# Kernel tuning notes

Measured on AMD Instinct MI355X. Metric: run time of the kernel, lower is better.

The kernel has to match this reference:

```python
import jax, jax.numpy as jnp
import numpy as np
from jax import lax

NB_W = 8  # weight bits
NB_A = 8  # activation bits
BN_EPS = 1e-3


def quant_weight(w, bits=NB_W):
    # symmetric per-tensor weight quantization with straight-through estimator
    qmax = 2.0 ** (bits - 1) - 1.0
    scale = jnp.max(jnp.abs(w)) / qmax
    wq = jnp.clip(jnp.round(w / scale), -qmax, qmax) * scale
    return w + lax.stop_gradient(wq - w)


def act_quant(x, alpha, bits=NB_A):
    # PACT-style: clip to [0, alpha], uniform quantize to 2^bits-1 levels, STE on round
    qmax = 2.0 ** bits - 1.0
    a = alpha.reshape(())
    xc = jnp.clip(x, 0.0, a)
    s = a / qmax
    xq = jnp.round(xc / s) * s
    return xc + lax.stop_gradient(xq - xc)


def bn_eval(x, gamma, beta, mean, var):
    inv = gamma / jnp.sqrt(var + BN_EPS)
    return x * inv[None, :, None, None] + (beta - mean * inv)[None, :, None, None]


def conv2d(x, w):
    return lax.conv_general_dilated(x, w, (1, 1), 'VALID',
                                    dimension_numbers=('NCHW', 'OIHW', 'NCHW'))


def setup_inputs() -> dict:
    ks = jax.random.split(jax.random.key(0), 8)
    B, C, H, W = 256, 768, 17, 17
    inp = {
        'act': jax.random.normal(ks[0], (B, C, H, W), jnp.float32),
        'alpha_in': jnp.ones((1,), jnp.float32),
        'conv0_w': jax.random.normal(ks[1], (128, 768, 1, 1), jnp.float32) * 0.05,
        'bn0_gamma': jnp.ones((128,), jnp.float32),
        'bn0_beta': jnp.zeros((128,), jnp.float32),
        'bn0_mean': jnp.zeros((128,), jnp.float32),
        'bn0_var': jnp.ones((128,), jnp.float32),
        'alpha0': jnp.full((1,), 8.0, jnp.float32),
        'conv1_w': jax.random.normal(ks[2], (768, 128, 5, 5), jnp.float32) * 0.01,
        'bn1_gamma': jnp.ones((768,), jnp.float32),
        'bn1_beta': jnp.zeros((768,), jnp.float32),
        'bn1_mean': jnp.zeros((768,), jnp.float32),
        'bn1_var': jnp.ones((768,), jnp.float32),
        'alpha1': jnp.full((1,), 8.0, jnp.float32),
        'fc_w': jax.random.normal(ks[3], (1000, 768), jnp.float32) * 0.001,
        'fc_b': jnp.zeros((1000,), jnp.float32),
    }
    return inp


def reference(act, alpha_in, conv0_w, bn0_gamma, bn0_beta, bn0_mean, bn0_var, alpha0,
              conv1_w, bn1_gamma, bn1_beta, bn1_mean, bn1_var, alpha1, fc_w, fc_b):
    # avg_pool k=5 s=3 VALID: 17x17 -> 5x5
    x = lax.reduce_window(act, 0.0, lax.add, (1, 1, 5, 5), (1, 1, 3, 3), 'VALID') / 25.0
    # conv0: quantized 1x1 conv 768->128, BN, ReLU, ACT_Q
    x = conv2d(x, quant_weight(conv0_w))
    x = jax.nn.relu(bn_eval(x, bn0_gamma, bn0_beta, bn0_mean, bn0_var))
    x = act_quant(x, alpha0)
    # conv1: quantized 5x5 conv 128->768 on 5x5 -> 1x1, BN, ReLU, ACT_Q
    x = conv2d(x, quant_weight(conv1_w))
    x = jax.nn.relu(bn_eval(x, bn1_gamma, bn1_beta, bn1_mean, bn1_var))
    x = act_quant(x, alpha1)
    # adaptive avg pool to 1x1 (already 1x1) + flatten
    x = jnp.mean(x, axis=(2, 3))  # [B, 768]
    # quantized linear head
    return x @ quant_weight(fc_w).T + fc_b
```

## Files before the change

kernel.cpp:

```cpp
#include <hip/hip_runtime.h>

#define NB 256
#define NC 768
#define HW 289
#define NP 25
#define OC0 128
#define K1 3200
#define NO 1000
#define M0 6400

#define OFF_MX    0
#define OFF_W0T   256
#define OFF_POOL  (OFF_W0T + 786432)
#define OFF_A0K   (OFF_POOL + 39321600)
#define OFF_W1R   (OFF_A0K + 819200)
#define OFF_SUMR1 (OFF_W1R + 2457600)
#define OFF_A1K   (OFF_SUMR1 + 4096)
#define OFF_FCR   (OFF_A1K + 196608)
#define OFF_SUMFC (OFF_FCR + 768000)

#if __has_builtin(__builtin_amdgcn_sdot4)
__device__ __forceinline__ int DOT4(unsigned a, unsigned b, int c) {
    return __builtin_amdgcn_sdot4((int)a, (int)b, c, false);
}
#else
__device__ __forceinline__ int DOT4(unsigned a, unsigned b, int c) {
    #pragma unroll
    for (int q = 0; q < 4; ++q)
        c += (int)(char)(a >> (8*q)) * (int)(char)(b >> (8*q));
    return c;
}
#endif

__global__ void k_init(unsigned* mx) {
    if (threadIdx.x < 3) mx[threadIdx.x] = 0u;
}

__global__ void k_absmax(const float* __restrict__ w, int n, unsigned* __restrict__ out) {
    float m = 0.f;
    for (int i = blockIdx.x * blockDim.x + threadIdx.x; i < n; i += gridDim.x * blockDim.x)
        m = fmaxf(m, fabsf(w[i]));
    #pragma unroll
    for (int off = 32; off; off >>= 1) m = fmaxf(m, __shfl_down(m, off));
    __shared__ float sm[4];
    if ((threadIdx.x & 63) == 0) sm[threadIdx.x >> 6] = m;
    __syncthreads();
    if (threadIdx.x == 0)
        atomicMax(out, __float_as_uint(fmaxf(fmaxf(sm[0], sm[1]), fmaxf(sm[2], sm[3]))));
}

__global__ void k_qw0t(const float* __restrict__ w, const float* __restrict__ mx,
                       double* __restrict__ out) {
    int i = blockIdx.x * 256 + threadIdx.x;
    double scale = (double)mx[0] / 127.0;
    int ic = i >> 7, oc = i & 127;
    double r = rint((double)w[oc * 768 + ic] / scale);
    r = fmin(fmax(r, -127.0), 127.0);
    out[i] = r * scale;
}

__global__ __launch_bounds__(256) void k_qwrow(const float* __restrict__ w, int rowlen,
                                               const float* __restrict__ mx, int mxi,
                                               char* __restrict__ out, int* __restrict__ sumr) {
    int row = blockIdx.x;
    double scale = (double)mx[mxi] / 127.0;
    const float* wr = w + (size_t)row * rowlen;
    char* orow = out + (size_t)row * rowlen;
    int s = 0;
    for (int t = threadIdx.x; t < rowlen; t += 256) {
        double r = rint((double)wr[t] / scale);
        r = fmin(fmax(r, -127.0), 127.0);
        int ri = (int)r;
        s += ri;
        orow[t] = (char)ri;
    }
    #pragma unroll
    for (int off = 32; off; off >>= 1) s += __shfl_down(s, off);
    __shared__ int sm[4];
    if ((threadIdx.x & 63) == 0) sm[threadIdx.x >> 6] = s;
    __syncthreads();
    if (threadIdx.x == 0) sumr[row] = sm[0] + sm[1] + sm[2] + sm[3];
}

__global__ __launch_bounds__(256) void k_pool(const float* __restrict__ x,
                                              double* __restrict__ pool_t) {
    __shared__ float tile[8 * HW];
    int g = blockIdx.x;
    int b = g / 96, icg = g % 96;
    const float* src = x + (size_t)g * (8 * HW);
    for (int i = threadIdx.x; i < 8 * HW; i += 256) tile[i] = src[i];
    __syncthreads();
    int t = threadIdx.x;
    if (t < 200) {
        int p = t >> 3, pl = t & 7;
        int oh = p / 5, ow = p % 5;
        const float* tp = tile + pl * HW + oh * 51 + ow * 3;
        double s = 0.0;
        #pragma unroll
        for (int kh = 0; kh < 5; ++kh)
            #pragma unroll
            for (int kw = 0; kw < 5; ++kw) s += (double)tp[kh * 17 + kw];
        pool_t[((size_t)b * NP + p) * NC + icg * 8 + pl] = s / 25.0;
    }
}

__global__ __launch_bounds__(256) void k_conv0(const double* __restrict__ A,
                                               const double* __restrict__ w0t,
                                               const float* __restrict__ g,
                                               const float* __restrict__ be,
                                               const float* __restrict__ mn,
                                               const float* __restrict__ vr,
                                               const float* __restrict__ alpha,
                                               char* __restrict__ a0k) {
    __shared__ double As[32][16];
    __shared__ double Bs[16][128];
    int m0 = blockIdx.x * 32;
    int tid = threadIdx.x;
    int ty = tid >> 5, tx = tid & 31;
    double acc[4][4] = {};
    for (int k0 = 0; k0 < NC; k0 += 16) {
        #pragma unroll
        for (int l = 0; l < 2; ++l) {
            int e = tid + l * 256;
            As[e >> 4][e & 15] = A[(size_t)(m0 + (e >> 4)) * NC + k0 + (e & 15)];
        }
        #pragma unroll
        for (int l = 0; l < 8; ++l) {
            int e = tid + l * 256;
            Bs[e >> 7][e & 127] = w0t[(size_t)(k0 + (e >> 7)) * OC0 + (e & 127)];
        }
        __syncthreads();
        #pragma unroll
        for (int kk = 0; kk < 16; ++kk) {
            double av[4], bv[4];
            #pragma unroll
            for (int i = 0; i < 4; ++i) av[i] = As[ty * 4 + i][kk];
            #pragma unroll
            for (int j = 0; j < 4; ++j) bv[j] = Bs[kk][tx + 32 * j];
            #pragma unroll
            for (int i = 0; i < 4; ++i)
                #pragma unroll
                for (int j = 0; j < 4; ++j)
                    acc[i][j] += av[i] * bv[j];
        }
        __syncthreads();
    }
    double a = (double)alpha[0];
    double s = a / 255.0;
    #pragma unroll
    for (int j = 0; j < 4; ++j) {
        int oc = tx + 32 * j;
        double inv = (double)g[oc] / sqrt((double)vr[oc] + 1e-3);
        double sh = (double)be[oc] - (double)mn[oc] * inv;
        #pragma unroll
        for (int i = 0; i < 4; ++i) {
            int r = m0 + ty * 4 + i;
            int b = r / 25, p = r % 25;
            double y = acc[i][j] * inv + sh;
            y = fmax(y, 0.0); y = fmin(y, a);
            int k = (int)rint(y / s);
            a0k[(size_t)b * K1 + oc * 25 + p] = (char)(k - 128);
        }
    }
}

__global__ __launch_bounds__(256) void k_conv1(const char* __restrict__ a0k,
                                               const char* __restrict__ w1r,
                                               const int* __restrict__ sumr,
                                               const float* __restrict__ g,
                                               const float* __restrict__ be,
                                               const float* __restrict__ mn,
                                               const float* __restrict__ vr,
                                               const float* __restrict__ alpha0,
                                               const float* __restrict__ alpha1,
                                               const float* __restrict__ mx,
                                               char* __restrict__ a1k) {
    __shared__ unsigned As[32][17];
    __shared__ unsigned Bs[32][17];
    int b0 = blockIdx.x * 32, oc0 = blockIdx.y * 32;
    int tid = threadIdx.x;
    int ty = tid >> 4, tx = tid & 15;
    int acc[2][2] = {};
    for (int k0 = 0; k0 < K1; k0 += 64) {
        int row = tid >> 3, o8 = (tid & 7) * 8;
        uint2 va = *(const uint2*)(a0k + (size_t)(b0 + row) * K1 + k0 + o8);
        As[row][o8 >> 2] = va.x; As[row][(o8 >> 2) + 1] = va.y;
        uint2 vb = *(const uint2*)(w1r + (size_t)(oc0 + row) * K1 + k0 + o8);
        Bs[row][o8 >> 2] = vb.x; Bs[row][(o8 >> 2) + 1] = vb.y;
        __syncthreads();
        #pragma unroll
        for (int kd = 0; kd < 16; ++kd) {
            unsigned av[2], bv[2];
            av[0] = As[ty * 2][kd];     av[1] = As[ty * 2 + 1][kd];
            bv[0] = Bs[tx * 2][kd];     bv[1] = Bs[tx * 2 + 1][kd];
            #pragma unroll
            for (int i = 0; i < 2; ++i)
                #pragma unroll
                for (int j = 0; j < 2; ++j)
                    acc[i][j] = DOT4(av[i], bv[j], acc[i][j]);
        }
        __syncthreads();
    }
    double s_a0 = (double)alpha0[0] / 255.0;
    double s_w1 = (double)mx[1] / 127.0;
    double m = s_a0 * s_w1;
    double a = (double)alpha1[0];
    double s1 = a / 255.0;
    #pragma unroll
    for (int j = 0; j < 2; ++j) {
        int oc = oc0 + tx * 2 + j;
        double inv = (double)g[oc] / sqrt((double)vr[oc] + 1e-3);
        double sh = (double)be[oc] - (double)mn[oc] * inv;
        int corr = 128 * sumr[oc];
        #pragma unroll
        for (int i = 0; i < 2; ++i) {
            int b = b0 + ty * 2 + i;
            double y = (double)(acc[i][j] + corr) * m * inv + sh;
            y = fmax(y, 0.0); y = fmin(y, a);
            int k = (int)rint(y / s1);
            a1k[(size_t)b * NC + oc] = (char)(k - 128);
        }
    }
}

__global__ __launch_bounds__(256) void k_fc(const char* __restrict__ a1k,
                                            const char* __restrict__ fcr,
                                            const int* __restrict__ sumr,
                                            const float* __restrict__ alpha1,
                                            const float* __restrict__ mx,
                                            const float* __restrict__ bias,
                                            float* __restrict__ out) {
    __shared__ unsigned As[32][17];
    __shared__ unsigned Bs[64][17];
    int b0 = blockIdx.x * 32, o0 = blockIdx.y * 64;
    int tid = threadIdx.x;
    int ry = tid >> 4, cx = tid & 15;
    int acc[2][4] = {};
    for (int k0 = 0; k0 < NC; k0 += 64) {
        {
            int row = tid >> 3, o8 = (tid & 7) * 8;
            uint2 va = *(const uint2*)(a1k + (size_t)(b0 + row) * NC + k0 + o8);
            As[row][o8 >> 2] = va.x; As[row][(o8 >> 2) + 1] = va.y;
        }
        {
            int row = tid >> 2, o16 = (tid & 3) * 16;
            uint4 vb = make_uint4(0u, 0u, 0u, 0u);
            if (o0 + row < NO)
                vb = *(const uint4*)(fcr + (size_t)(o0 + row) * NC + k0 + o16);
            Bs[row][o16 >> 2] = vb.x; Bs[row][(o16 >> 2) + 1] = vb.y;
            Bs[row][(o16 >> 2) + 2] = vb.z; Bs[row][(o16 >> 2) + 3] = vb.w;
        }
        __syncthreads();
        #pragma unroll
        for (int kd = 0; kd < 16; ++kd) {
            unsigned av[2], bv[4];
            #pragma unroll
            for (int i = 0; i < 2; ++i) av[i] = As[ry * 2 + i][kd];
            #pragma unroll
            for (int j = 0; j < 4; ++j) bv[j] = Bs[cx * 4 + j][kd];
            #pragma unroll
            for (int i = 0; i < 2; ++i)
                #pragma unroll
                for (int j = 0; j < 4; ++j)
                    acc[i][j] = DOT4(av[i], bv[j], acc[i][j]);
        }
        __syncthreads();
    }
    double s_a1 = (double)alpha1[0] / 255.0;
    double s_fc = (double)mx[2] / 127.0;
    double m = s_a1 * s_fc;
    #pragma unroll
    for (int j = 0; j < 4; ++j) {
        int o = o0 + cx * 4 + j;
        if (o < NO) {
            int corr = 128 * sumr[o];
            double bi = (double)bias[o];
            #pragma unroll
            for (int i = 0; i < 2; ++i) {
                int b = b0 + ry * 2 + i;
                out[(size_t)b * NO + o] = (float)((double)(acc[i][j] + corr) * m + bi);
            }
        }
    }
}

extern "C" void kernel_launch(void* const* d_in, const int* in_sizes, int n_in,
                              void* d_out, int out_size, void* d_ws, size_t ws_size,
                              hipStream_t stream) {
    const float* act     = (const float*)d_in[0];
    const float* conv0_w = (const float*)d_in[2];
    const float* bn0g = (const float*)d_in[3];
    const float* bn0b = (const float*)d_in[4];
    const float* bn0m = (const float*)d_in[5];
    const float* bn0v = (const float*)d_in[6];
    const float* alpha0 = (const float*)d_in[7];
    const float* conv1_w = (const float*)d_in[8];
    const float* bn1g = (const float*)d_in[9];
    const float* bn1b = (const float*)d_in[10];
    const float* bn1m = (const float*)d_in[11];
    const float* bn1v = (const float*)d_in[12];
    const float* alpha1 = (const float*)d_in[13];
    const float* fc_w = (const float*)d_in[14];
    const float* fc_b = (const float*)d_in[15];

    char* base = (char*)d_ws;
    unsigned* mxu = (unsigned*)(base + OFF_MX);
    const float* mxf = (const float*)(base + OFF_MX);
    double* w0t  = (double*)(base + OFF_W0T);
    double* poolt= (double*)(base + OFF_POOL);
    char* a0k    = (char*)(base + OFF_A0K);
    char* w1r    = (char*)(base + OFF_W1R);
    int* sumr1   = (int*)(base + OFF_SUMR1);
    char* a1k    = (char*)(base + OFF_A1K);
    char* fcr    = (char*)(base + OFF_FCR);
    int* sumfc   = (int*)(base + OFF_SUMFC);
    float* out   = (float*)d_out;

    k_init<<<1, 64, 0, stream>>>(mxu);
    k_absmax<<<256, 256, 0, stream>>>(conv0_w, 98304, mxu + 0);
    k_absmax<<<256, 256, 0, stream>>>(conv1_w, 2457600, mxu + 1);
    k_absmax<<<256, 256, 0, stream>>>(fc_w, 768000, mxu + 2);

    k_qw0t<<<384, 256, 0, stream>>>(conv0_w, mxf, w0t);
    k_qwrow<<<768, 256, 0, stream>>>(conv1_w, K1, mxf, 1, w1r, sumr1);
    k_qwrow<<<1000, 256, 0, stream>>>(fc_w, NC, mxf, 2, fcr, sumfc);

    k_pool<<<24576, 256, 0, stream>>>(act, poolt);
    k_conv0<<<200, 256, 0, stream>>>(poolt, w0t, bn0g, bn0b, bn0m, bn0v, alpha0, a0k);
    k_conv1<<<dim3(8, 24), 256, 0, stream>>>(a0k, w1r, sumr1, bn1g, bn1b, bn1m, bn1v,
                                             alpha0, alpha1, mxf, a1k);
    k_fc<<<dim3(8, 16), 256, 0, stream>>>(a1k, fcr, sumfc, alpha1, mxf, fc_b, out);
}
```

Measured before the change: 573.4 us.

## Split-K conv1 and fc GEMMs, retile conv0, store pooled activations as float

The conv1 and fc integer GEMMs now split K across a third grid dimension and write partial sums to workspace. New epilogue kernels add the partials and apply the BN, quantisation and bias steps. conv0 is retiled into smaller tiles over a 2D grid to raise the block count, and the pooled intermediate is stored as float instead of double to halve its traffic. The cost is extra partial-sum traffic and two more launches, plus rounding risk from the float pooled values feeding the conv0 quantisation.

```diff
diff --git a/kernel.cpp b/kernel.cpp
--- a/kernel.cpp
+++ b/kernel.cpp
@@ -12,12 +12,14 @@
 #define OFF_MX    0
 #define OFF_W0T   256
 #define OFF_POOL  (OFF_W0T + 786432)
-#define OFF_A0K   (OFF_POOL + 39321600)
+#define OFF_A0K   (OFF_POOL + 19660800)
 #define OFF_W1R   (OFF_A0K + 819200)
 #define OFF_SUMR1 (OFF_W1R + 2457600)
 #define OFF_A1K   (OFF_SUMR1 + 4096)
 #define OFF_FCR   (OFF_A1K + 196608)
 #define OFF_SUMFC (OFF_FCR + 768000)
+#define OFF_P1    (OFF_SUMFC + 4096)
+#define OFF_PFC   (OFF_P1 + 3932160)
 
 #if __has_builtin(__builtin_amdgcn_sdot4)
 __device__ __forceinline__ int DOT4(unsigned a, unsigned b, int c) {
@@ -83,7 +85,7 @@
 }
 
 __global__ __launch_bounds__(256) void k_pool(const float* __restrict__ x,
-                                              double* __restrict__ pool_t) {
+                                              float* __restrict__ pool_t) {
     __shared__ float tile[8 * HW];
     int g = blockIdx.x;
     int b = g / 96, icg = g % 96;
@@ -100,11 +102,11 @@
         for (int kh = 0; kh < 5; ++kh)
             #pragma unroll
             for (int kw = 0; kw < 5; ++kw) s += (double)tp[kh * 17 + kw];
-        pool_t[((size_t)b * NP + p) * NC + icg * 8 + pl] = s / 25.0;
-    }
-}
-
-__global__ __launch_bounds__(256) void k_conv0(const double* __restrict__ A,
+        pool_t[((size_t)b * NP + p) * NC + icg * 8 + pl] = (float)(s / 25.0);
+    }
+}
+
+__global__ __launch_bounds__(256) void k_conv0(const float* __restrict__ A,
                                                const double* __restrict__ w0t,
                                                const float* __restrict__ g,
                                                const float* __restrict__ be,
@@ -112,50 +114,48 @@
                                                const float* __restrict__ vr,
                                                const float* __restrict__ alpha,
                                                char* __restrict__ a0k) {
-    __shared__ double As[32][16];
-    __shared__ double Bs[16][128];
-    int m0 = blockIdx.x * 32;
+    __shared__ double Ast[32][18];
+    __shared__ double Bs[32][65];
+    int m0 = blockIdx.x * 16;
+    int oc0 = blockIdx.y * 64;
     int tid = threadIdx.x;
     int ty = tid >> 5, tx = tid & 31;
-    double acc[4][4] = {};
-    for (int k0 = 0; k0 < NC; k0 += 16) {
-        #pragma unroll
-        for (int l = 0; l < 2; ++l) {
+    double acc[2][2] = {};
+    for (int k0 = 0; k0 < NC; k0 += 32) {
+        {
+            int r = tid >> 4, kk2 = (tid & 15) * 2;
+            float2 v = *(const float2*)(A + (size_t)(m0 + r) * NC + k0 + kk2);
+            Ast[kk2][r] = (double)v.x;
+            Ast[kk2 + 1][r] = (double)v.y;
+        }
+        #pragma unroll
+        for (int l = 0; l < 4; ++l) {
             int e = tid + l * 256;
-            As[e >> 4][e & 15] = A[(size_t)(m0 + (e >> 4)) * NC + k0 + (e & 15)];
-        }
-        #pragma unroll
-        for (int l = 0; l < 8; ++l) {
-            int e = tid + l * 256;
-            Bs[e >> 7][e & 127] = w0t[(size_t)(k0 + (e >> 7)) * OC0 + (e & 127)];
-        }
-        __syncthreads();
-        #pragma unroll
-        for (int kk = 0; kk < 16; ++kk) {
-            double av[4], bv[4];
-            #pragma unroll
-            for (int i = 0; i < 4; ++i) av[i] = As[ty * 4 + i][kk];
-            #pragma unroll
-            for (int j = 0; j < 4; ++j) bv[j] = Bs[kk][tx + 32 * j];
-            #pragma unroll
-            for (int i = 0; i < 4; ++i)
-                #pragma unroll
-                for (int j = 0; j < 4; ++j)
-                    acc[i][j] += av[i] * bv[j];
+            int r = e >> 5, c2 = (e & 31) * 2;
+            double2 v = *(const double2*)(w0t + (size_t)(k0 + r) * OC0 + oc0 + c2);
+            Bs[r][c2] = v.x; Bs[r][c2 + 1] = v.y;
+        }
+        __syncthreads();
+        #pragma unroll
+        for (int kk = 0; kk < 32; ++kk) {
+            double av0 = Ast[kk][ty * 2], av1 = Ast[kk][ty * 2 + 1];
+            double bv0 = Bs[kk][tx], bv1 = Bs[kk][tx + 32];
+            acc[0][0] += av0 * bv0; acc[0][1] += av0 * bv1;
+            acc[1][0] += av1 * bv0; acc[1][1] += av1 * bv1;
         }
         __syncthreads();
     }
     double a = (double)alpha[0];
     double s = a / 255.0;
     #pragma unroll
-    for (int j = 0; j < 4; ++j) {
-        int oc = tx + 32 * j;
+    for (int j = 0; j < 2; ++j) {
+        int oc = oc0 + tx + 32 * j;
         double inv = (double)g[oc] / sqrt((double)vr[oc] + 1e-3);
         double sh = (double)be[oc] - (double)mn[oc] * inv;
         #pragma unroll
-        for (int i = 0; i < 4; ++i) {
-            int r = m0 + ty * 4 + i;
-            int b = r / 25, p = r % 25;
+        for (int i = 0; i < 2; ++i) {
+            int m = m0 + ty * 2 + i;
+            int b = m / 25, p = m % 25;
             double y = acc[i][j] * inv + sh;
             y = fmax(y, 0.0); y = fmin(y, a);
             int k = (int)rint(y / s);
@@ -166,22 +166,15 @@
 
 __global__ __launch_bounds__(256) void k_conv1(const char* __restrict__ a0k,
                                                const char* __restrict__ w1r,
-                                               const int* __restrict__ sumr,
-                                               const float* __restrict__ g,
-                                               const float* __restrict__ be,
-                                               const float* __restrict__ mn,
-                                               const float* __restrict__ vr,
-                                               const float* __restrict__ alpha0,
-                                               const float* __restrict__ alpha1,
-                                               const float* __restrict__ mx,
-                                               char* __restrict__ a1k) {
+                                               int* __restrict__ part) {
     __shared__ unsigned As[32][17];
     __shared__ unsigned Bs[32][17];
     int b0 = blockIdx.x * 32, oc0 = blockIdx.y * 32;
+    int kbeg = blockIdx.z * 640;
     int tid = threadIdx.x;
     int ty = tid >> 4, tx = tid & 15;
     int acc[2][2] = {};
-    for (int k0 = 0; k0 < K1; k0 += 64) {
+    for (int k0 = kbeg; k0 < kbeg + 640; k0 += 64) {
         int row = tid >> 3, o8 = (tid & 7) * 8;
         uint2 va = *(const uint2*)(a0k + (size_t)(b0 + row) * K1 + k0 + o8);
         As[row][o8 >> 2] = va.x; As[row][(o8 >> 2) + 1] = va.y;
@@ -201,42 +194,51 @@
         }
         __syncthreads();
     }
-    double s_a0 = (double)alpha0[0] / 255.0;
-    double s_w1 = (double)mx[1] / 127.0;
-    double m = s_a0 * s_w1;
+    int* pp = part + (size_t)blockIdx.z * (NB * NC);
+    #pragma unroll
+    for (int i = 0; i < 2; ++i)
+        #pragma unroll
+        for (int j = 0; j < 2; ++j)
+            pp[(size_t)(b0 + ty * 2 + i) * NC + oc0 + tx * 2 + j] = acc[i][j];
+}
+
+__global__ __launch_bounds__(256) void k_bnq1(const int* __restrict__ part,
+                                              const int* __restrict__ sumr,
+                                              const float* __restrict__ g,
+                                              const float* __restrict__ be,
+                                              const float* __restrict__ mn,
+                                              const float* __restrict__ vr,
+                                              const float* __restrict__ alpha0,
+                                              const float* __restrict__ alpha1,
+                                              const float* __restrict__ mx,
+                                              char* __restrict__ a1k) {
+    int t = blockIdx.x * 256 + threadIdx.x;
+    int oc = t % NC;
+    int s = 128 * sumr[oc];
+    #pragma unroll
+    for (int kz = 0; kz < 5; ++kz) s += part[(size_t)kz * (NB * NC) + t];
+    double m = ((double)alpha0[0] / 255.0) * ((double)mx[1] / 127.0);
+    double inv = (double)g[oc] / sqrt((double)vr[oc] + 1e-3);
+    double sh = (double)be[oc] - (double)mn[oc] * inv;
     double a = (double)alpha1[0];
     double s1 = a / 255.0;
-    #pragma unroll
-    for (int j = 0; j < 2; ++j) {
-        int oc = oc0 + tx * 2 + j;
-        double inv = (double)g[oc] / sqrt((double)vr[oc] + 1e-3);
-        double sh = (double)be[oc] - (double)mn[oc] * inv;
-        int corr = 128 * sumr[oc];
-        #pragma unroll
-        for (int i = 0; i < 2; ++i) {
-            int b = b0 + ty * 2 + i;
-            double y = (double)(acc[i][j] + corr) * m * inv + sh;
-            y = fmax(y, 0.0); y = fmin(y, a);
-            int k = (int)rint(y / s1);
-            a1k[(size_t)b * NC + oc] = (char)(k - 128);
-        }
-    }
+    double y = (double)s * m * inv + sh;
+    y = fmax(y, 0.0); y = fmin(y, a);
+    int k = (int)rint(y / s1);
+    a1k[t] = (char)(k - 128);
 }
 
 __global__ __launch_bounds__(256) void k_fc(const char* __restrict__ a1k,
                                             const char* __restrict__ fcr,
-                                            const int* __restrict__ sumr,
-                                            const float* __restrict__ alpha1,
-                                            const float* __restrict__ mx,
-                                            const float* __restrict__ bias,
-                                            float* __restrict__ out) {
+                                            int* __restrict__ part) {
     __shared__ unsigned As[32][17];
     __shared__ unsigned Bs[64][17];
     int b0 = blockIdx.x * 32, o0 = blockIdx.y * 64;
+    int kbeg = blockIdx.z * 384;
     int tid = threadIdx.x;
     int ry = tid >> 4, cx = tid & 15;
     int acc[2][4] = {};
-    for (int k0 = 0; k0 < NC; k0 += 64) {
+    for (int k0 = kbeg; k0 < kbeg + 384; k0 += 64) {
         {
             int row = tid >> 3, o8 = (tid & 7) * 8;
             uint2 va = *(const uint2*)(a1k + (size_t)(b0 + row) * NC + k0 + o8);
@@ -266,22 +268,28 @@
         }
         __syncthreads();
     }
-    double s_a1 = (double)alpha1[0] / 255.0;
-    double s_fc = (double)mx[2] / 127.0;
-    double m = s_a1 * s_fc;
+    int* pp = part + (size_t)blockIdx.z * (NB * NO);
     #pragma unroll
     for (int j = 0; j < 4; ++j) {
         int o = o0 + cx * 4 + j;
-        if (o < NO) {
-            int corr = 128 * sumr[o];
-            double bi = (double)bias[o];
-            #pragma unroll
-            for (int i = 0; i < 2; ++i) {
-                int b = b0 + ry * 2 + i;
-                out[(size_t)b * NO + o] = (float)((double)(acc[i][j] + corr) * m + bi);
-            }
-        }
-    }
+        if (o < NO)
+            #pragma unroll
+            for (int i = 0; i < 2; ++i)
+                pp[(size_t)(b0 + ry * 2 + i) * NO + o] = acc[i][j];
+    }
+}
+
+__global__ __launch_bounds__(256) void k_out(const int* __restrict__ part,
+                                             const int* __restrict__ sumr,
+                                             const float* __restrict__ alpha1,
+                                             const float* __restrict__ mx,
+                                             const float* __restrict__ bias,
+                                             float* __restrict__ out) {
+    int t = blockIdx.x * 256 + threadIdx.x;
+    int o = t % NO;
+    int s = 128 * sumr[o] + part[t] + part[(size_t)(NB * NO) + t];
+    double m = ((double)alpha1[0] / 255.0) * ((double)mx[2] / 127.0);
+    out[t] = (float)((double)s * m + (double)bias[o]);
 }
 
 extern "C" void kernel_launch(void* const* d_in, const int* in_sizes, int n_in,
@@ -307,13 +315,15 @@
     unsigned* mxu = (unsigned*)(base + OFF_MX);
     const float* mxf = (const float*)(base + OFF_MX);
     double* w0t  = (double*)(base + OFF_W0T);
-    double* poolt= (double*)(base + OFF_POOL);
+    float* poolt = (float*)(base + OFF_POOL);
     char* a0k    = (char*)(base + OFF_A0K);
     char* w1r    = (char*)(base + OFF_W1R);
     int* sumr1   = (int*)(base + OFF_SUMR1);
     char* a1k    = (char*)(base + OFF_A1K);
     char* fcr    = (char*)(base + OFF_FCR);
     int* sumfc   = (int*)(base + OFF_SUMFC);
+    int* part1   = (int*)(base + OFF_P1);
+    int* partfc  = (int*)(base + OFF_PFC);
     float* out   = (float*)d_out;
 
     k_init<<<1, 64, 0, stream>>>(mxu);
@@ -326,8 +336,11 @@
     k_qwrow<<<1000, 256, 0, stream>>>(fc_w, NC, mxf, 2, fcr, sumfc);
 
     k_pool<<<24576, 256, 0, stream>>>(act, poolt);
-    k_conv0<<<200, 256, 0, stream>>>(poolt, w0t, bn0g, bn0b, bn0m, bn0v, alpha0, a0k);
-    k_conv1<<<dim3(8, 24), 256, 0, stream>>>(a0k, w1r, sumr1, bn1g, bn1b, bn1m, bn1v,
-                                             alpha0, alpha1, mxf, a1k);
-    k_fc<<<dim3(8, 16), 256, 0, stream>>>(a1k, fcr, sumfc, alpha1, mxf, fc_b, out);
-}
+    k_conv0<<<dim3(400, 2), 256, 0, stream>>>(poolt, w0t, bn0g, bn0b, bn0m, bn0v,
+                                              alpha0, a0k);
+    k_conv1<<<dim3(8, 24, 5), 256, 0, stream>>>(a0k, w1r, part1);
+    k_bnq1<<<768, 256, 0, stream>>>(part1, sumr1, bn1g, bn1b, bn1m, bn1v,
+                                    alpha0, alpha1, mxf, a1k);
+    k_fc<<<dim3(8, 16, 2), 256, 0, stream>>>(a1k, fcr, partfc);
+    k_out<<<1000, 256, 0, stream>>>(partfc, sumfc, alpha1, mxf, fc_b, out);
+}
```

New measurement: 527.7 us. 8.0% less time.
